# Optimization experiments

Measured on AMD Instinct MI355X. Metric: run time of the kernel, lower is better.

## Reference

```python
import jax, jax.numpy as jnp
import numpy as np

DIM = 192
HEADS = 6
HSP = 8
WSP = 8
POS_DIM = (DIM // 4) // 4  # 12


def _ln(x, g, b, eps=1e-5):
    m = jnp.mean(x, -1, keepdims=True)
    v = jnp.mean((x - m) ** 2, -1, keepdims=True)
    return (x - m) / jnp.sqrt(v + eps) * g + b


def _rel_tables():
    # rpe_biases: ((2*HSP-1)*(2*WSP-1), 2) float coords of all relative offsets
    bh, bw = np.meshgrid(np.arange(1 - HSP, HSP), np.arange(1 - WSP, WSP), indexing='ij')
    biases = np.stack([bh, bw], -1).reshape(-1, 2).astype(np.float32)
    # relative_position_index: (N, N) int lookup into the bias table
    ch, cw = np.meshgrid(np.arange(HSP), np.arange(WSP), indexing='ij')
    coords = np.stack([ch, cw], 0).reshape(2, -1)  # (2, N)
    rel = coords[:, :, None] - coords[:, None, :]  # (2, N, N)
    idx = (rel[0] + HSP - 1) * (2 * WSP - 1) + (rel[1] + WSP - 1)
    return jnp.asarray(biases), jnp.asarray(idx.astype(np.int32))


def setup_inputs() -> dict:
    key = jax.random.key(0)
    ks = jax.random.split(key, 8)
    B, H, W = 2, 256, 256
    L = H * W
    def lin(k, i, o):
        return jax.random.normal(k, (i, o), jnp.float32) * 0.02
    return {
        'qkv': jax.random.normal(ks[0], (3, B, L, DIM), jnp.float32),
        'w_proj': lin(ks[1], 2, POS_DIM), 'b_proj': jnp.zeros((POS_DIM,), jnp.float32),
        'g1': jnp.ones((POS_DIM,), jnp.float32), 'be1': jnp.zeros((POS_DIM,), jnp.float32),
        'w1': lin(ks[2], POS_DIM, POS_DIM), 'b1': jnp.zeros((POS_DIM,), jnp.float32),
        'g2': jnp.ones((POS_DIM,), jnp.float32), 'be2': jnp.zeros((POS_DIM,), jnp.float32),
        'w2': lin(ks[3], POS_DIM, POS_DIM), 'b2': jnp.zeros((POS_DIM,), jnp.float32),
        'g3': jnp.ones((POS_DIM,), jnp.float32), 'be3': jnp.zeros((POS_DIM,), jnp.float32),
        'w3': lin(ks[4], POS_DIM, HEADS), 'b3': jnp.zeros((HEADS,), jnp.float32),
        'H': H, 'W': W,
    }


def reference(qkv, w_proj, b_proj, g1, be1, w1, b1, g2, be2, w2, b2, g3, be3, w3, b3, H, W):
    B, L, C = qkv.shape[1], qkv.shape[2], qkv.shape[3]
    hd = C // HEADS
    scale = float(hd) ** -0.5
    N = HSP * WSP

    def im2win(x):
        # (B, L, C) -> (B*nW, heads, N, hd)
        x = x.reshape(B, H // HSP, HSP, W // WSP, WSP, C)
        x = x.transpose(0, 1, 3, 2, 4, 5).reshape(-1, N, HEADS, hd)
        return x.transpose(0, 2, 1, 3)

    q = im2win(qkv[0]) * scale
    k = im2win(qkv[1])
    v = im2win(qkv[2])

    attn = jnp.einsum('whnd,whmd->whnm', q, k)  # (B*nW, heads, N, N)

    # dynamic relative position bias via MLP (DynamicPosBias, residual=False)
    biases, rel_idx = _rel_tables()
    p = biases @ w_proj + b_proj
    p = jax.nn.relu(_ln(p, g1, be1)) @ w1 + b1
    p = jax.nn.relu(_ln(p, g2, be2)) @ w2 + b2
    p = jax.nn.relu(_ln(p, g3, be3)) @ w3 + b3  # (n_rel, heads)
    rpb = p[rel_idx.reshape(-1)].reshape(N, N, HEADS).transpose(2, 0, 1)  # (heads, N, N)
    attn = attn + rpb[None]

    attn = jax.nn.softmax(attn, axis=-1)
    x = jnp.einsum('whnm,whmd->whnd', attn, v)  # (B*nW, heads, N, hd)
    x = x.transpose(0, 2, 1, 3).reshape(-1, N, C)

    # windows2img: (B*nW, N, C) -> (B, H, W, C)
    x = x.reshape(B, H // HSP, W // WSP, HSP, WSP, C)
    x = x.transpose(0, 1, 3, 2, 4, 5).reshape(B, H, W, C)
    return x
```

## Files before the change

kernel.cpp:

```cpp
#include <hip/hip_runtime.h>
#include <hip/hip_bf16.h>

#define NHEADS 6
#define HD 32
#define CDIM 192
#define NTOK 64
#define NREL 225
#define PDIM 12
#define IMG 256
#define NWIN 2048
#define QSCALE 0.2550348686f
#define LOG2E 1.4426950408889634f

typedef __attribute__((ext_vector_type(8))) short v8s;
typedef __attribute__((ext_vector_type(4))) float v4f;

#define KS3 104
#define VTS 72

__device__ __forceinline__ unsigned pkbf(float x, float y) {
    __hip_bfloat162 h = __float22bfloat162_rn(make_float2(x, y));
    union { __hip_bfloat162 h; unsigned u; } c; c.h = h;
    return c.u;
}

__device__ __forceinline__ float ex2(float x) {
    float r; asm("v_exp_f32 %0, %1" : "=v"(r) : "v"(x)); return r;
}

__device__ __forceinline__ void ln_relu12(const float* x, const float* g,
                                          const float* be, float* y) {
    float m = 0.f;
#pragma unroll
    for (int i = 0; i < PDIM; ++i) m += x[i];
    m *= (1.f / PDIM);
    float v = 0.f;
#pragma unroll
    for (int i = 0; i < PDIM; ++i) { float d = x[i] - m; v += d * d; }
    v *= (1.f / PDIM);
    float inv = rsqrtf(v + 1e-5f);
#pragma unroll
    for (int i = 0; i < PDIM; ++i) {
        float t = (x[i] - m) * inv * g[i] + be[i];
        y[i] = t > 0.f ? t : 0.f;
    }
}

__global__ __launch_bounds__(256, 4) void win_attn_fused(
    const float* __restrict__ qkv,
    const float* __restrict__ wp, const float* __restrict__ bp,
    const float* __restrict__ g1, const float* __restrict__ be1,
    const float* __restrict__ w1, const float* __restrict__ b1,
    const float* __restrict__ g2, const float* __restrict__ be2,
    const float* __restrict__ w2, const float* __restrict__ b2,
    const float* __restrict__ g3, const float* __restrict__ be3,
    const float* __restrict__ w3, const float* __restrict__ b3,
    float* __restrict__ out)
{
    __shared__ __align__(16) unsigned short ks[NTOK * KS3];
    __shared__ __align__(16) unsigned short vt[96 * VTS];
    __shared__ __align__(16) float pshf[NREL * 4];

    const int t = threadIdx.x;
    const int bid = blockIdx.x;
    const int win = bid >> 1;
    const int hg  = bid & 1;
    const int b  = win >> 10;
    const int bh = (win >> 5) & 31;
    const int bw = win & 31;

    const int lane = t & 63;
    const int rg   = t >> 6;
    const int lw = lane & 15;
    const int lg = lane >> 4;
    const int rowbase = rg * 16;
    const int hoff = hg * 96;

    const size_t PL = (size_t)2 * IMG * IMG * CDIM;
    const float* qplane = qkv + (size_t)b * IMG * IMG * CDIM;
    const float* kplane = qplane + PL;
    const float* vplane = kplane + PL;

    auto pixoff = [&](int tok) -> size_t {
        return ((size_t)(bh * 8 + (tok >> 3)) * IMG + (bw * 8 + (tok & 7))) * CDIM;
    };

    float4 kreg[6];
    int kpix[6], kf[6];
#pragma unroll
    for (int pass = 0; pass < 6; ++pass) {
        int fidx = t + pass * 256;
        int pix = fidx / 24;
        int f   = fidx - pix * 24;
        kreg[pass] = *(const float4*)(kplane + pixoff(pix) + hoff + f * 4);
        kpix[pass] = pix; kf[pass] = f;
    }
#pragma unroll
    for (int pass = 0; pass < 6; ++pass) {
        uint2 kk;
        kk.x = pkbf(kreg[pass].x, kreg[pass].y);
        kk.y = pkbf(kreg[pass].z, kreg[pass].w);
        *(uint2*)&ks[kpix[pass] * KS3 + kf[pass] * 4] = kk;
    }

    {
        const int tp = t & 31;
        const int g  = t >> 5;
        const int tok0 = 2 * tp;
        const int k0 = ((tok0 >> 5) << 5) + (((tok0 >> 2) & 3) << 3)
                     + (((tok0 >> 4) & 1) << 2) + (tok0 & 3);
        const size_t offa = pixoff(tok0) + hoff, offb = pixoff(tok0 + 1) + hoff;
#pragma unroll
        for (int i = 0; i < 3; ++i) {
            int f = g + i * 8;
            float4 vA = *(const float4*)(vplane + offa + f * 4);
            float4 vB = *(const float4*)(vplane + offb + f * 4);
            int d0 = f * 4;
            *(unsigned*)&vt[(d0 + 0) * VTS + k0] = pkbf(vA.x, vB.x);
            *(unsigned*)&vt[(d0 + 1) * VTS + k0] = pkbf(vA.y, vB.y);
            *(unsigned*)&vt[(d0 + 2) * VTS + k0] = pkbf(vA.z, vB.z);
            *(unsigned*)&vt[(d0 + 3) * VTS + k0] = pkbf(vA.w, vB.w);
        }
    }

    v8s aq[3];
    {
        const size_t qoff = pixoff(rowbase + lw) + hoff;
#pragma unroll
        for (int hi = 0; hi < 3; ++hi) {
            const float* qp = qplane + qoff + hi * HD + lg * 8;
            float4 q0 = *(const float4*)qp;
            float4 q1 = *(const float4*)(qp + 4);
            union { v8s v; unsigned x[4]; } au;
            au.x[0] = pkbf(q0.x * QSCALE, q0.y * QSCALE);
            au.x[1] = pkbf(q0.z * QSCALE, q0.w * QSCALE);
            au.x[2] = pkbf(q1.x * QSCALE, q1.y * QSCALE);
            au.x[3] = pkbf(q1.z * QSCALE, q1.w * QSCALE);
            aq[hi] = au.v;
        }
    }

    if (t < NREL) {
        float x0 = (float)(t / 15 - 7);
        float x1 = (float)(t % 15 - 7);
        float h[PDIM], y[PDIM];
#pragma unroll
        for (int o = 0; o < PDIM; ++o)
            h[o] = x0 * wp[o] + x1 * wp[PDIM + o] + bp[o];
        ln_relu12(h, g1, be1, y);
#pragma unroll
        for (int o = 0; o < PDIM; ++o) {
            float a = b1[o];
#pragma unroll
            for (int i = 0; i < PDIM; ++i) a += y[i] * w1[i * PDIM + o];
            h[o] = a;
        }
        ln_relu12(h, g2, be2, y);
#pragma unroll
        for (int o = 0; o < PDIM; ++o) {
            float a = b2[o];
#pragma unroll
            for (int i = 0; i < PDIM; ++i) a += y[i] * w2[i * PDIM + o];
            h[o] = a;
        }
        ln_relu12(h, g3, be3, y);
#pragma unroll
        for (int hi = 0; hi < 3; ++hi) {
            int o = hg * 3 + hi;
            float a = b3[o];
#pragma unroll
            for (int i = 0; i < PDIM; ++i) a += y[i] * w3[i * NHEADS + o];
            pshf[t * 4 + hi] = a * LOG2E;
        }
    }
    __syncthreads();

    v4f acc[3][4];
#pragma unroll
    for (int ct = 0; ct < 4; ++ct) {
#pragma unroll
        for (int hi = 0; hi < 3; ++hi) {
            v4f z = {0.f, 0.f, 0.f, 0.f};
            v8s bfr = *(const v8s*)&ks[(ct * 16 + lw) * KS3 + hi * HD + lg * 8];
            acc[hi][ct] = __builtin_amdgcn_mfma_f32_16x16x32_bf16(bfr, aq[hi], z, 0, 0, 0);
        }
    }

    {
        const int q = rowbase + lw;
        const int base2 = ((q >> 3) + 7) * 15 + (q & 7) + 7
                        - ((lg >> 1) * 15 + (lg & 1) * 4);
#pragma unroll
        for (int ct = 0; ct < 4; ++ct)
#pragma unroll
            for (int r = 0; r < 4; ++r) {
                int idx = base2 - ct * 30 - r;
                const float4 bb = *(const float4*)&pshf[idx * 4];
                acc[0][ct][r] = ex2(acc[0][ct][r] + bb.x);
                acc[1][ct][r] = ex2(acc[1][ct][r] + bb.y);
                acc[2][ct][r] = ex2(acc[2][ct][r] + bb.z);
            }
    }

    unsigned pa[3][2][4];
#pragma unroll
    for (int hi = 0; hi < 3; ++hi) {
        float s = 0.f;
#pragma unroll
        for (int ct = 0; ct < 4; ++ct)
#pragma unroll
            for (int r = 0; r < 4; ++r) s += acc[hi][ct][r];
        s += __shfl_xor(s, 16);
        s += __shfl_xor(s, 32);
        float rv = __builtin_amdgcn_rcpf(s);
#pragma unroll
        for (int kt = 0; kt < 2; ++kt) {
            pa[hi][kt][0] = pkbf(acc[hi][2*kt][0] * rv, acc[hi][2*kt][1] * rv);
            pa[hi][kt][1] = pkbf(acc[hi][2*kt][2] * rv, acc[hi][2*kt][3] * rv);
            pa[hi][kt][2] = pkbf(acc[hi][2*kt+1][0] * rv, acc[hi][2*kt+1][1] * rv);
            pa[hi][kt][3] = pkbf(acc[hi][2*kt+1][2] * rv, acc[hi][2*kt+1][3] * rv);
        }
    }

    size_t ooff[4];
#pragma unroll
    for (int r = 0; r < 4; ++r) {
        int n = rowbase + lg * 4 + r;
        ooff[r] = ((size_t)(b * IMG + bh * 8 + (n >> 3)) * IMG
                   + (bw * 8 + (n & 7))) * CDIM;
    }

#pragma unroll
    for (int hi = 0; hi < 3; ++hi) {
        v4f acc2[2] = {};
#pragma unroll
        for (int kt = 0; kt < 2; ++kt) {
            v8s pav = *(const v8s*)&pa[hi][kt][0];
#pragma unroll
            for (int dt = 0; dt < 2; ++dt) {
                v8s vb = *(const v8s*)&vt[(hi * HD + dt * 16 + lw) * VTS
                                          + kt * 32 + lg * 8];
                acc2[dt] = __builtin_amdgcn_mfma_f32_16x16x32_bf16(pav, vb, acc2[dt], 0, 0, 0);
            }
        }
        const int h = hg * 3 + hi;
#pragma unroll
        for (int dt = 0; dt < 2; ++dt)
#pragma unroll
            for (int r = 0; r < 4; ++r)
                out[ooff[r] + h * HD + dt * 16 + lw] = acc2[dt][r];
    }
}

extern "C" void kernel_launch(void* const* d_in, const int* in_sizes, int n_in,
                              void* d_out, int out_size, void* d_ws, size_t ws_size,
                              hipStream_t stream) {
    const float* qkv = (const float*)d_in[0];
    win_attn_fused<<<NWIN * 2, 256, 0, stream>>>(
        qkv,
        (const float*)d_in[1], (const float*)d_in[2],
        (const float*)d_in[3], (const float*)d_in[4],
        (const float*)d_in[5], (const float*)d_in[6],
        (const float*)d_in[7], (const float*)d_in[8],
        (const float*)d_in[9], (const float*)d_in[10],
        (const float*)d_in[11], (const float*)d_in[12],
        (const float*)d_in[13], (const float*)d_in[14],
        (float*)d_out);
}
```

Before: 84.39 us.

## Split work to one head per block with 128-thread blocks

Changes the decomposition from two blocks per window, each handling three heads with four waves, to six blocks per window, each handling one head with two waves that each cover 32 query rows. Each wave reuses its K fragment across two query subtiles and preloads the V fragments once, and shared memory shrinks to one head's K, V and bias table. This buys more blocks and occupancy and less LDS per block, but every block now recomputes the whole relative-position MLP (225 entries with two waves), so that redundant work triples.

New measurement: 173.4 us. 2.05x slower.

```diff
diff --git a/kernel.cpp b/kernel.cpp
--- a/kernel.cpp
+++ b/kernel.cpp
@@ -15,7 +15,7 @@
 typedef __attribute__((ext_vector_type(8))) short v8s;
 typedef __attribute__((ext_vector_type(4))) float v4f;
 
-#define KS3 104
+#define KS 40
 #define VTS 72
 
 __device__ __forceinline__ unsigned pkbf(float x, float y) {
@@ -46,7 +46,7 @@
     }
 }
 
-__global__ __launch_bounds__(256, 4) void win_attn_fused(
+__global__ __launch_bounds__(128, 4) void win_attn_fused(
     const float* __restrict__ qkv,
     const float* __restrict__ wp, const float* __restrict__ bp,
     const float* __restrict__ g1, const float* __restrict__ be1,
@@ -57,24 +57,24 @@
     const float* __restrict__ w3, const float* __restrict__ b3,
     float* __restrict__ out)
 {
-    __shared__ __align__(16) unsigned short ks[NTOK * KS3];
-    __shared__ __align__(16) unsigned short vt[96 * VTS];
-    __shared__ __align__(16) float pshf[NREL * 4];
+    __shared__ __align__(16) unsigned short ks[NTOK * KS];
+    __shared__ __align__(16) unsigned short vt[HD * VTS];
+    __shared__ float psh[NREL];
 
     const int t = threadIdx.x;
     const int bid = blockIdx.x;
-    const int win = bid >> 1;
-    const int hg  = bid & 1;
+    const int win = bid / NHEADS;
+    const int head = bid - win * NHEADS;
     const int b  = win >> 10;
     const int bh = (win >> 5) & 31;
     const int bw = win & 31;
 
     const int lane = t & 63;
-    const int rg   = t >> 6;
+    const int wave = t >> 6;
     const int lw = lane & 15;
     const int lg = lane >> 4;
-    const int rowbase = rg * 16;
-    const int hoff = hg * 96;
+    const int rowbase = wave * 32;
+    const int hoff = head * HD;
 
     const size_t PL = (size_t)2 * IMG * IMG * CDIM;
     const float* qplane = qkv + (size_t)b * IMG * IMG * CDIM;
@@ -85,22 +85,14 @@
         return ((size_t)(bh * 8 + (tok >> 3)) * IMG + (bw * 8 + (tok & 7))) * CDIM;
     };
 
-    float4 kreg[6];
-    int kpix[6], kf[6];
-#pragma unroll
-    for (int pass = 0; pass < 6; ++pass) {
-        int fidx = t + pass * 256;
-        int pix = fidx / 24;
-        int f   = fidx - pix * 24;
-        kreg[pass] = *(const float4*)(kplane + pixoff(pix) + hoff + f * 4);
-        kpix[pass] = pix; kf[pass] = f;
-    }
-#pragma unroll
-    for (int pass = 0; pass < 6; ++pass) {
-        uint2 kk;
-        kk.x = pkbf(kreg[pass].x, kreg[pass].y);
-        kk.y = pkbf(kreg[pass].z, kreg[pass].w);
-        *(uint2*)&ks[kpix[pass] * KS3 + kf[pass] * 4] = kk;
+#pragma unroll
+    for (int pass = 0; pass < 4; ++pass) {
+        int fidx = t + pass * 128;
+        int pix = fidx >> 3;
+        int f   = fidx & 7;
+        float4 k4 = *(const float4*)(kplane + pixoff(pix) + hoff + f * 4);
+        uint2 kk; kk.x = pkbf(k4.x, k4.y); kk.y = pkbf(k4.z, k4.w);
+        *(uint2*)&ks[pix * KS + f * 4] = kk;
     }
 
     {
@@ -111,8 +103,8 @@
                      + (((tok0 >> 4) & 1) << 2) + (tok0 & 3);
         const size_t offa = pixoff(tok0) + hoff, offb = pixoff(tok0 + 1) + hoff;
 #pragma unroll
-        for (int i = 0; i < 3; ++i) {
-            int f = g + i * 8;
+        for (int i = 0; i < 2; ++i) {
+            int f = g + i * 4;
             float4 vA = *(const float4*)(vplane + offa + f * 4);
             float4 vB = *(const float4*)(vplane + offb + f * 4);
             int d0 = f * 4;
@@ -123,26 +115,23 @@
         }
     }
 
-    v8s aq[3];
-    {
-        const size_t qoff = pixoff(rowbase + lw) + hoff;
-#pragma unroll
-        for (int hi = 0; hi < 3; ++hi) {
-            const float* qp = qplane + qoff + hi * HD + lg * 8;
-            float4 q0 = *(const float4*)qp;
-            float4 q1 = *(const float4*)(qp + 4);
-            union { v8s v; unsigned x[4]; } au;
-            au.x[0] = pkbf(q0.x * QSCALE, q0.y * QSCALE);
-            au.x[1] = pkbf(q0.z * QSCALE, q0.w * QSCALE);
-            au.x[2] = pkbf(q1.x * QSCALE, q1.y * QSCALE);
-            au.x[3] = pkbf(q1.z * QSCALE, q1.w * QSCALE);
-            aq[hi] = au.v;
-        }
-    }
-
-    if (t < NREL) {
-        float x0 = (float)(t / 15 - 7);
-        float x1 = (float)(t % 15 - 7);
+    v8s aq[2];
+#pragma unroll
+    for (int s = 0; s < 2; ++s) {
+        const float* qp = qplane + pixoff(rowbase + s * 16 + lw) + hoff + lg * 8;
+        float4 q0 = *(const float4*)qp;
+        float4 q1 = *(const float4*)(qp + 4);
+        union { v8s v; unsigned x[4]; } au;
+        au.x[0] = pkbf(q0.x * QSCALE, q0.y * QSCALE);
+        au.x[1] = pkbf(q0.z * QSCALE, q0.w * QSCALE);
+        au.x[2] = pkbf(q1.x * QSCALE, q1.y * QSCALE);
+        au.x[3] = pkbf(q1.z * QSCALE, q1.w * QSCALE);
+        aq[s] = au.v;
+    }
+
+    for (int rr = t; rr < NREL; rr += 128) {
+        float x0 = (float)(rr / 15 - 7);
+        float x1 = (float)(rr % 15 - 7);
         float h[PDIM], y[PDIM];
 #pragma unroll
         for (int o = 0; o < PDIM; ++o)
@@ -164,91 +153,82 @@
             h[o] = a;
         }
         ln_relu12(h, g3, be3, y);
-#pragma unroll
-        for (int hi = 0; hi < 3; ++hi) {
-            int o = hg * 3 + hi;
-            float a = b3[o];
-#pragma unroll
-            for (int i = 0; i < PDIM; ++i) a += y[i] * w3[i * NHEADS + o];
-            pshf[t * 4 + hi] = a * LOG2E;
-        }
+        float a = b3[head];
+#pragma unroll
+        for (int i = 0; i < PDIM; ++i) a += y[i] * w3[i * NHEADS + head];
+        psh[rr] = a * LOG2E;
     }
     __syncthreads();
 
-    v4f acc[3][4];
+    v4f acc[2][4];
 #pragma unroll
     for (int ct = 0; ct < 4; ++ct) {
-#pragma unroll
-        for (int hi = 0; hi < 3; ++hi) {
+        v8s bfr = *(const v8s*)&ks[(ct * 16 + lw) * KS + lg * 8];
+#pragma unroll
+        for (int s = 0; s < 2; ++s) {
             v4f z = {0.f, 0.f, 0.f, 0.f};
-            v8s bfr = *(const v8s*)&ks[(ct * 16 + lw) * KS3 + hi * HD + lg * 8];
-            acc[hi][ct] = __builtin_amdgcn_mfma_f32_16x16x32_bf16(bfr, aq[hi], z, 0, 0, 0);
-        }
-    }
-
-    {
-        const int q = rowbase + lw;
+            acc[s][ct] = __builtin_amdgcn_mfma_f32_16x16x32_bf16(bfr, aq[s], z, 0, 0, 0);
+        }
+    }
+
+#pragma unroll
+    for (int s = 0; s < 2; ++s) {
+        const int q = rowbase + s * 16 + lw;
         const int base2 = ((q >> 3) + 7) * 15 + (q & 7) + 7
                         - ((lg >> 1) * 15 + (lg & 1) * 4);
 #pragma unroll
         for (int ct = 0; ct < 4; ++ct)
 #pragma unroll
-            for (int r = 0; r < 4; ++r) {
-                int idx = base2 - ct * 30 - r;
-                const float4 bb = *(const float4*)&pshf[idx * 4];
-                acc[0][ct][r] = ex2(acc[0][ct][r] + bb.x);
-                acc[1][ct][r] = ex2(acc[1][ct][r] + bb.y);
-                acc[2][ct][r] = ex2(acc[2][ct][r] + bb.z);
-            }
-    }
-
-    unsigned pa[3][2][4];
-#pragma unroll
-    for (int hi = 0; hi < 3; ++hi) {
-        float s = 0.f;
+            for (int r = 0; r < 4; ++r)
+                acc[s][ct][r] = ex2(acc[s][ct][r] + psh[base2 - ct * 30 - r]);
+    }
+
+    unsigned pa[2][2][4];
+#pragma unroll
+    for (int s = 0; s < 2; ++s) {
+        float sum = 0.f;
 #pragma unroll
         for (int ct = 0; ct < 4; ++ct)
 #pragma unroll
-            for (int r = 0; r < 4; ++r) s += acc[hi][ct][r];
-        s += __shfl_xor(s, 16);
-        s += __shfl_xor(s, 32);
-        float rv = __builtin_amdgcn_rcpf(s);
+            for (int r = 0; r < 4; ++r) sum += acc[s][ct][r];
+        sum += __shfl_xor(sum, 16);
+        sum += __shfl_xor(sum, 32);
+        float rv = __builtin_amdgcn_rcpf(sum);
 #pragma unroll
         for (int kt = 0; kt < 2; ++kt) {
-            pa[hi][kt][0] = pkbf(acc[hi][2*kt][0] * rv, acc[hi][2*kt][1] * rv);
-            pa[hi][kt][1] = pkbf(acc[hi][2*kt][2] * rv, acc[hi][2*kt][3] * rv);
-            pa[hi][kt][2] = pkbf(acc[hi][2*kt+1][0] * rv, acc[hi][2*kt+1][1] * rv);
-            pa[hi][kt][3] = pkbf(acc[hi][2*kt+1][2] * rv, acc[hi][2*kt+1][3] * rv);
-        }
-    }
-
-    size_t ooff[4];
-#pragma unroll
-    for (int r = 0; r < 4; ++r) {
-        int n = rowbase + lg * 4 + r;
-        ooff[r] = ((size_t)(b * IMG + bh * 8 + (n >> 3)) * IMG
-                   + (bw * 8 + (n & 7))) * CDIM;
-    }
-
-#pragma unroll
-    for (int hi = 0; hi < 3; ++hi) {
+            pa[s][kt][0] = pkbf(acc[s][2*kt][0] * rv, acc[s][2*kt][1] * rv);
+            pa[s][kt][1] = pkbf(acc[s][2*kt][2] * rv, acc[s][2*kt][3] * rv);
+            pa[s][kt][2] = pkbf(acc[s][2*kt+1][0] * rv, acc[s][2*kt+1][1] * rv);
+            pa[s][kt][3] = pkbf(acc[s][2*kt+1][2] * rv, acc[s][2*kt+1][3] * rv);
+        }
+    }
+
+    v8s vbr[2][2];
+#pragma unroll
+    for (int kt = 0; kt < 2; ++kt)
+#pragma unroll
+        for (int dt = 0; dt < 2; ++dt)
+            vbr[kt][dt] = *(const v8s*)&vt[(dt * 16 + lw) * VTS + kt * 32 + lg * 8];
+
+#pragma unroll
+    for (int s = 0; s < 2; ++s) {
         v4f acc2[2] = {};
 #pragma unroll
         for (int kt = 0; kt < 2; ++kt) {
-            v8s pav = *(const v8s*)&pa[hi][kt][0];
-#pragma unroll
-            for (int dt = 0; dt < 2; ++dt) {
-                v8s vb = *(const v8s*)&vt[(hi * HD + dt * 16 + lw) * VTS
-                                          + kt * 32 + lg * 8];
-                acc2[dt] = __builtin_amdgcn_mfma_f32_16x16x32_bf16(pav, vb, acc2[dt], 0, 0, 0);
-            }
-        }
-        const int h = hg * 3 + hi;
-#pragma unroll
-        for (int dt = 0; dt < 2; ++dt)
-#pragma unroll
-            for (int r = 0; r < 4; ++r)
-                out[ooff[r] + h * HD + dt * 16 + lw] = acc2[dt][r];
+            v8s pav = *(const v8s*)&pa[s][kt][0];
+#pragma unroll
+            for (int dt = 0; dt < 2; ++dt)
+                acc2[dt] = __builtin_amdgcn_mfma_f32_16x16x32_bf16(pav, vbr[kt][dt], acc2[dt], 0, 0, 0);
+        }
+#pragma unroll
+        for (int r = 0; r < 4; ++r) {
+            int n = rowbase + s * 16 + lg * 4 + r;
+            size_t ooff = ((size_t)(b * IMG + bh * 8 + (n >> 3)) * IMG
+                           + (bw * 8 + (n & 7))) * CDIM + hoff;
+#pragma unroll
+            for (int dt = 0; dt < 2; ++dt)
+                out[ooff + dt * 16 + lw] = acc2[dt][r];
+        }
     }
 }
 
@@ -256,7 +236,7 @@
                               void* d_out, int out_size, void* d_ws, size_t ws_size,
                               hipStream_t stream) {
     const float* qkv = (const float*)d_in[0];
-    win_attn_fused<<<NWIN * 2, 256, 0, stream>>>(
+    win_attn_fused<<<NWIN * NHEADS, 128, 0, stream>>>(
         qkv,
         (const float*)d_in[1], (const float*)d_in[2],
         (const float*)d_in[3], (const float*)d_in[4],
```

## Process two windows per block with register-prefetched second window

Applied to the files above, without the earlier changes.

Each block now handles two windows for one head group, halving the grid and reusing the bias-MLP result across both windows. The second window's K and V are loaded into registers before the first window's compute and written to a second shared-memory buffer afterwards, so their global load latency overlaps with the first window's compute. This costs more registers (launch bounds lowered from 4 to 2 blocks per CU), double shared buffers, and fewer blocks, which reduces occupancy and parallelism.

New measurement: 93.50 us. +10.8%, slower.

```diff
diff --git a/kernel.cpp b/kernel.cpp
--- a/kernel.cpp
+++ b/kernel.cpp
@@ -46,9 +46,9 @@
     }
 }
 
-__global__ __launch_bounds__(256, 4) void win_attn_fused(
+__global__ __launch_bounds__(256, 2) void win_attn_fused(
     const float* __restrict__ qkv,
-    const float* __restrict__ wp, const float* __restrict__ bp,
+    const float* __restrict__ wpj, const float* __restrict__ bp,
     const float* __restrict__ g1, const float* __restrict__ be1,
     const float* __restrict__ w1, const float* __restrict__ b1,
     const float* __restrict__ g2, const float* __restrict__ be2,
@@ -57,78 +57,72 @@
     const float* __restrict__ w3, const float* __restrict__ b3,
     float* __restrict__ out)
 {
-    __shared__ __align__(16) unsigned short ks[NTOK * KS3];
-    __shared__ __align__(16) unsigned short vt[96 * VTS];
+    __shared__ __align__(16) unsigned short ks[2][NTOK * KS3];
+    __shared__ __align__(16) unsigned short vt[2][96 * VTS];
     __shared__ __align__(16) float pshf[NREL * 4];
 
     const int t = threadIdx.x;
     const int bid = blockIdx.x;
-    const int win = bid >> 1;
-    const int hg  = bid & 1;
-    const int b  = win >> 10;
-    const int bh = (win >> 5) & 31;
-    const int bw = win & 31;
+    const int hg    = bid >> 10;
+    const int wpair = bid & 1023;
+    const int hoff = hg * 96;
 
     const int lane = t & 63;
     const int rg   = t >> 6;
     const int lw = lane & 15;
     const int lg = lane >> 4;
     const int rowbase = rg * 16;
-    const int hoff = hg * 96;
+
+    const int win0 = wpair * 2, win1 = wpair * 2 + 1;
+    const int bat0 = win0 >> 10, bh0 = (win0 >> 5) & 31, bw0 = win0 & 31;
+    const int bat1 = win1 >> 10, bh1 = (win1 >> 5) & 31, bw1 = win1 & 31;
 
     const size_t PL = (size_t)2 * IMG * IMG * CDIM;
-    const float* qplane = qkv + (size_t)b * IMG * IMG * CDIM;
-    const float* kplane = qplane + PL;
-    const float* vplane = kplane + PL;
-
-    auto pixoff = [&](int tok) -> size_t {
+    const float* qpl0 = qkv + (size_t)bat0 * IMG * IMG * CDIM;
+    const float* qpl1 = qkv + (size_t)bat1 * IMG * IMG * CDIM;
+
+    auto pixoff = [&](int bh, int bw, int tok) -> size_t {
         return ((size_t)(bh * 8 + (tok >> 3)) * IMG + (bw * 8 + (tok & 7))) * CDIM;
     };
 
-    float4 kreg[6];
-    int kpix[6], kf[6];
+    const int tp = t & 31;
+    const int vg = t >> 5;
+    const int tok0 = 2 * tp;
+    const int k0 = ((tok0 >> 5) << 5) + (((tok0 >> 2) & 3) << 3)
+                 + (((tok0 >> 4) & 1) << 2) + (tok0 & 3);
+
 #pragma unroll
     for (int pass = 0; pass < 6; ++pass) {
         int fidx = t + pass * 256;
         int pix = fidx / 24;
         int f   = fidx - pix * 24;
-        kreg[pass] = *(const float4*)(kplane + pixoff(pix) + hoff + f * 4);
-        kpix[pass] = pix; kf[pass] = f;
-    }
-#pragma unroll
-    for (int pass = 0; pass < 6; ++pass) {
-        uint2 kk;
-        kk.x = pkbf(kreg[pass].x, kreg[pass].y);
-        kk.y = pkbf(kreg[pass].z, kreg[pass].w);
-        *(uint2*)&ks[kpix[pass] * KS3 + kf[pass] * 4] = kk;
-    }
-
+        float4 k4 = *(const float4*)(qpl0 + PL + pixoff(bh0, bw0, pix) + hoff + f * 4);
+        uint2 kk; kk.x = pkbf(k4.x, k4.y); kk.y = pkbf(k4.z, k4.w);
+        *(uint2*)&ks[0][pix * KS3 + f * 4] = kk;
+    }
     {
-        const int tp = t & 31;
-        const int g  = t >> 5;
-        const int tok0 = 2 * tp;
-        const int k0 = ((tok0 >> 5) << 5) + (((tok0 >> 2) & 3) << 3)
-                     + (((tok0 >> 4) & 1) << 2) + (tok0 & 3);
-        const size_t offa = pixoff(tok0) + hoff, offb = pixoff(tok0 + 1) + hoff;
+        const size_t offa = pixoff(bh0, bw0, tok0) + hoff;
+        const size_t offb = pixoff(bh0, bw0, tok0 + 1) + hoff;
 #pragma unroll
         for (int i = 0; i < 3; ++i) {
-            int f = g + i * 8;
-            float4 vA = *(const float4*)(vplane + offa + f * 4);
-            float4 vB = *(const float4*)(vplane + offb + f * 4);
+            int f = vg + i * 8;
+            float4 vA = *(const float4*)(qpl0 + 2 * PL + offa + f * 4);
+            float4 vB = *(const float4*)(qpl0 + 2 * PL + offb + f * 4);
             int d0 = f * 4;
-            *(unsigned*)&vt[(d0 + 0) * VTS + k0] = pkbf(vA.x, vB.x);
-            *(unsigned*)&vt[(d0 + 1) * VTS + k0] = pkbf(vA.y, vB.y);
-            *(unsigned*)&vt[(d0 + 2) * VTS + k0] = pkbf(vA.z, vB.z);
-            *(unsigned*)&vt[(d0 + 3) * VTS + k0] = pkbf(vA.w, vB.w);
-        }
-    }
-
-    v8s aq[3];
+            *(unsigned*)&vt[0][(d0 + 0) * VTS + k0] = pkbf(vA.x, vB.x);
+            *(unsigned*)&vt[0][(d0 + 1) * VTS + k0] = pkbf(vA.y, vB.y);
+            *(unsigned*)&vt[0][(d0 + 2) * VTS + k0] = pkbf(vA.z, vB.z);
+            *(unsigned*)&vt[0][(d0 + 3) * VTS + k0] = pkbf(vA.w, vB.w);
+        }
+    }
+
+    v8s aq0[3], aq1[3];
     {
-        const size_t qoff = pixoff(rowbase + lw) + hoff;
+        const size_t qo0 = pixoff(bh0, bw0, rowbase + lw) + hoff;
+        const size_t qo1 = pixoff(bh1, bw1, rowbase + lw) + hoff;
 #pragma unroll
         for (int hi = 0; hi < 3; ++hi) {
-            const float* qp = qplane + qoff + hi * HD + lg * 8;
+            const float* qp = qpl0 + qo0 + hi * HD + lg * 8;
             float4 q0 = *(const float4*)qp;
             float4 q1 = *(const float4*)(qp + 4);
             union { v8s v; unsigned x[4]; } au;
@@ -136,7 +130,35 @@
             au.x[1] = pkbf(q0.z * QSCALE, q0.w * QSCALE);
             au.x[2] = pkbf(q1.x * QSCALE, q1.y * QSCALE);
             au.x[3] = pkbf(q1.z * QSCALE, q1.w * QSCALE);
-            aq[hi] = au.v;
+            aq0[hi] = au.v;
+            const float* qq = qpl1 + qo1 + hi * HD + lg * 8;
+            float4 p0 = *(const float4*)qq;
+            float4 p1 = *(const float4*)(qq + 4);
+            au.x[0] = pkbf(p0.x * QSCALE, p0.y * QSCALE);
+            au.x[1] = pkbf(p0.z * QSCALE, p0.w * QSCALE);
+            au.x[2] = pkbf(p1.x * QSCALE, p1.y * QSCALE);
+            au.x[3] = pkbf(p1.z * QSCALE, p1.w * QSCALE);
+            aq1[hi] = au.v;
+        }
+    }
+
+    float4 kreg[6];
+#pragma unroll
+    for (int pass = 0; pass < 6; ++pass) {
+        int fidx = t + pass * 256;
+        int pix = fidx / 24;
+        int f   = fidx - pix * 24;
+        kreg[pass] = *(const float4*)(qpl1 + PL + pixoff(bh1, bw1, pix) + hoff + f * 4);
+    }
+    float4 vA1[3], vB1[3];
+    {
+        const size_t offa = pixoff(bh1, bw1, tok0) + hoff;
+        const size_t offb = pixoff(bh1, bw1, tok0 + 1) + hoff;
+#pragma unroll
+        for (int i = 0; i < 3; ++i) {
+            int f = vg + i * 8;
+            vA1[i] = *(const float4*)(qpl1 + 2 * PL + offa + f * 4);
+            vB1[i] = *(const float4*)(qpl1 + 2 * PL + offb + f * 4);
         }
     }
 
@@ -146,7 +168,7 @@
         float h[PDIM], y[PDIM];
 #pragma unroll
         for (int o = 0; o < PDIM; ++o)
-            h[o] = x0 * wp[o] + x1 * wp[PDIM + o] + bp[o];
+            h[o] = x0 * wpj[o] + x1 * wpj[PDIM + o] + bp[o];
         ln_relu12(h, g1, be1, y);
 #pragma unroll
         for (int o = 0; o < PDIM; ++o) {
@@ -175,18 +197,17 @@
     }
     __syncthreads();
 
-    v4f acc[3][4];
-#pragma unroll
-    for (int ct = 0; ct < 4; ++ct) {
-#pragma unroll
-        for (int hi = 0; hi < 3; ++hi) {
-            v4f z = {0.f, 0.f, 0.f, 0.f};
-            v8s bfr = *(const v8s*)&ks[(ct * 16 + lw) * KS3 + hi * HD + lg * 8];
-            acc[hi][ct] = __builtin_amdgcn_mfma_f32_16x16x32_bf16(bfr, aq[hi], z, 0, 0, 0);
-        }
-    }
-
-    {
+    auto compute_store = [&](const unsigned short* ksb, const unsigned short* vtb,
+                             const v8s* aq, int batt, int bhh, int bww) {
+        v4f acc[3][4];
+#pragma unroll
+        for (int ct = 0; ct < 4; ++ct)
+#pragma unroll
+            for (int hi = 0; hi < 3; ++hi) {
+                v4f z = {0.f, 0.f, 0.f, 0.f};
+                v8s bfr = *(const v8s*)&ksb[(ct * 16 + lw) * KS3 + hi * HD + lg * 8];
+                acc[hi][ct] = __builtin_amdgcn_mfma_f32_16x16x32_bf16(bfr, aq[hi], z, 0, 0, 0);
+            }
         const int q = rowbase + lw;
         const int base2 = ((q >> 3) + 7) * 15 + (q & 7) + 7
                         - ((lg >> 1) * 15 + (lg & 1) * 4);
@@ -200,63 +221,84 @@
                 acc[1][ct][r] = ex2(acc[1][ct][r] + bb.y);
                 acc[2][ct][r] = ex2(acc[2][ct][r] + bb.z);
             }
-    }
-
-    unsigned pa[3][2][4];
-#pragma unroll
-    for (int hi = 0; hi < 3; ++hi) {
-        float s = 0.f;
-#pragma unroll
-        for (int ct = 0; ct < 4; ++ct)
-#pragma unroll
-            for (int r = 0; r < 4; ++r) s += acc[hi][ct][r];
-        s += __shfl_xor(s, 16);
-        s += __shfl_xor(s, 32);
-        float rv = __builtin_amdgcn_rcpf(s);
-#pragma unroll
-        for (int kt = 0; kt < 2; ++kt) {
-            pa[hi][kt][0] = pkbf(acc[hi][2*kt][0] * rv, acc[hi][2*kt][1] * rv);
-            pa[hi][kt][1] = pkbf(acc[hi][2*kt][2] * rv, acc[hi][2*kt][3] * rv);
-            pa[hi][kt][2] = pkbf(acc[hi][2*kt+1][0] * rv, acc[hi][2*kt+1][1] * rv);
-            pa[hi][kt][3] = pkbf(acc[hi][2*kt+1][2] * rv, acc[hi][2*kt+1][3] * rv);
-        }
-    }
-
-    size_t ooff[4];
-#pragma unroll
-    for (int r = 0; r < 4; ++r) {
-        int n = rowbase + lg * 4 + r;
-        ooff[r] = ((size_t)(b * IMG + bh * 8 + (n >> 3)) * IMG
-                   + (bw * 8 + (n & 7))) * CDIM;
-    }
-
-#pragma unroll
-    for (int hi = 0; hi < 3; ++hi) {
-        v4f acc2[2] = {};
-#pragma unroll
-        for (int kt = 0; kt < 2; ++kt) {
-            v8s pav = *(const v8s*)&pa[hi][kt][0];
-#pragma unroll
-            for (int dt = 0; dt < 2; ++dt) {
-                v8s vb = *(const v8s*)&vt[(hi * HD + dt * 16 + lw) * VTS
-                                          + kt * 32 + lg * 8];
-                acc2[dt] = __builtin_amdgcn_mfma_f32_16x16x32_bf16(pav, vb, acc2[dt], 0, 0, 0);
+        unsigned pa[3][2][4];
+#pragma unroll
+        for (int hi = 0; hi < 3; ++hi) {
+            float s = 0.f;
+#pragma unroll
+            for (int ct = 0; ct < 4; ++ct)
+#pragma unroll
+                for (int r = 0; r < 4; ++r) s += acc[hi][ct][r];
+            s += __shfl_xor(s, 16);
+            s += __shfl_xor(s, 32);
+            float rv = __builtin_amdgcn_rcpf(s);
+#pragma unroll
+            for (int kt = 0; kt < 2; ++kt) {
+                pa[hi][kt][0] = pkbf(acc[hi][2*kt][0] * rv, acc[hi][2*kt][1] * rv);
+                pa[hi][kt][1] = pkbf(acc[hi][2*kt][2] * rv, acc[hi][2*kt][3] * rv);
+                pa[hi][kt][2] = pkbf(acc[hi][2*kt+1][0] * rv, acc[hi][2*kt+1][1] * rv);
+                pa[hi][kt][3] = pkbf(acc[hi][2*kt+1][2] * rv, acc[hi][2*kt+1][3] * rv);
             }
         }
-        const int h = hg * 3 + hi;
-#pragma unroll
-        for (int dt = 0; dt < 2; ++dt)
-#pragma unroll
-            for (int r = 0; r < 4; ++r)
-                out[ooff[r] + h * HD + dt * 16 + lw] = acc2[dt][r];
-    }
+        size_t ooff[4];
+#pragma unroll
+        for (int r = 0; r < 4; ++r) {
+            int n = rowbase + lg * 4 + r;
+            ooff[r] = ((size_t)(batt * IMG + bhh * 8 + (n >> 3)) * IMG
+                       + (bww * 8 + (n & 7))) * CDIM;
+        }
+#pragma unroll
+        for (int hi = 0; hi < 3; ++hi) {
+            v4f acc2[2] = {};
+#pragma unroll
+            for (int kt = 0; kt < 2; ++kt) {
+                v8s pav = *(const v8s*)&pa[hi][kt][0];
+#pragma unroll
+                for (int dt = 0; dt < 2; ++dt) {
+                    v8s vb = *(const v8s*)&vtb[(hi * HD + dt * 16 + lw) * VTS
+                                               + kt * 32 + lg * 8];
+                    acc2[dt] = __builtin_amdgcn_mfma_f32_16x16x32_bf16(pav, vb, acc2[dt], 0, 0, 0);
+                }
+            }
+            const int h = hg * 3 + hi;
+#pragma unroll
+            for (int dt = 0; dt < 2; ++dt)
+#pragma unroll
+                for (int r = 0; r < 4; ++r)
+                    out[ooff[r] + h * HD + dt * 16 + lw] = acc2[dt][r];
+        }
+    };
+
+    compute_store(ks[0], vt[0], aq0, bat0, bh0, bw0);
+
+#pragma unroll
+    for (int pass = 0; pass < 6; ++pass) {
+        int fidx = t + pass * 256;
+        int pix = fidx / 24;
+        int f   = fidx - pix * 24;
+        uint2 kk;
+        kk.x = pkbf(kreg[pass].x, kreg[pass].y);
+        kk.y = pkbf(kreg[pass].z, kreg[pass].w);
+        *(uint2*)&ks[1][pix * KS3 + f * 4] = kk;
+    }
+#pragma unroll
+    for (int i = 0; i < 3; ++i) {
+        int d0 = (vg + i * 8) * 4;
+        *(unsigned*)&vt[1][(d0 + 0) * VTS + k0] = pkbf(vA1[i].x, vB1[i].x);
+        *(unsigned*)&vt[1][(d0 + 1) * VTS + k0] = pkbf(vA1[i].y, vB1[i].y);
+        *(unsigned*)&vt[1][(d0 + 2) * VTS + k0] = pkbf(vA1[i].z, vB1[i].z);
+        *(unsigned*)&vt[1][(d0 + 3) * VTS + k0] = pkbf(vA1[i].w, vB1[i].w);
+    }
+    __syncthreads();
+
+    compute_store(ks[1], vt[1], aq1, bat1, bh1, bw1);
 }
 
 extern "C" void kernel_launch(void* const* d_in, const int* in_sizes, int n_in,
                               void* d_out, int out_size, void* d_ws, size_t ws_size,
                               hipStream_t stream) {
     const float* qkv = (const float*)d_in[0];
-    win_attn_fused<<<NWIN * 2, 256, 0, stream>>>(
+    win_attn_fused<<<NWIN, 256, 0, stream>>>(
         qkv,
         (const float*)d_in[1], (const float*)d_in[2],
         (const float*)d_in[3], (const float*)d_in[4],
```
